# Optimization experiments

Hardware: AMD Instinct MI355X
Metric: run time of the kernel (lower is better)

The kernel has to match this reference:

```python
import jax, jax.numpy as jnp
from jax import lax
import numpy as np

B, L = 8, 2048
D_MODEL, D_STATE, D_CONV, EXPAND = 768, 16, 4, 2
D_INNER = EXPAND * D_MODEL          # 1536
DT_RANK = (D_MODEL + 15) // 16      # 48
OUT_DIM = 2


def setup_inputs() -> dict:
    key = jax.random.key(0)
    ks = jax.random.split(key, 10)
    rn = lambda k, sh, sc=0.02: jax.random.normal(k, sh, jnp.float32) * sc
    # S4D-real init for A_log, as in mamba_ssm
    A_log = jnp.log(jnp.broadcast_to(
        jnp.arange(1, D_STATE + 1, dtype=jnp.float32), (D_INNER, D_STATE)))
    return {
        "x": jax.random.normal(ks[0], (B, L, D_MODEL), jnp.float32),
        "in_proj_w": rn(ks[1], (2 * D_INNER, D_MODEL)),
        "conv_w": rn(ks[2], (D_INNER, D_CONV), 0.1),   # depthwise kernel
        "conv_b": jnp.zeros((D_INNER,), jnp.float32),
        "x_proj_w": rn(ks[3], (DT_RANK + 2 * D_STATE, D_INNER)),
        "dt_proj_w": rn(ks[4], (D_INNER, DT_RANK), 0.1),
        "dt_proj_b": rn(ks[5], (D_INNER,), 0.1),
        "A_log": A_log,
        "D": jnp.ones((D_INNER,), jnp.float32),
        "out_proj_w": rn(ks[6], (D_MODEL, D_INNER)),
        "fc_w": rn(ks[7], (OUT_DIM, D_MODEL)),
        "fc_b": jnp.zeros((OUT_DIM,), jnp.float32),
    }


def _mamba(x, in_proj_w, conv_w, conv_b, x_proj_w, dt_proj_w, dt_proj_b,
           A_log, D, out_proj_w):
    # input projection -> x branch and gate z, each [B, L, E]
    xz = jnp.einsum('bld,ed->ble', x, in_proj_w)
    xi, z = jnp.split(xz, 2, axis=-1)
    # causal depthwise conv1d over time, then SiLU
    xc = jnp.swapaxes(xi, 1, 2)                      # [B, E, L]
    xc = lax.conv_general_dilated(
        xc, conv_w[:, None, :], window_strides=(1,),
        padding=[(D_CONV - 1, 0)], feature_group_count=D_INNER)
    xi = jax.nn.silu(jnp.swapaxes(xc + conv_b[None, :, None], 1, 2))  # [B,L,E]
    # input-dependent dt, B, C
    dbc = jnp.einsum('ble,fe->blf', xi, x_proj_w)    # [B, L, R+2N]
    dt, Bm, Cm = jnp.split(dbc, [DT_RANK, DT_RANK + D_STATE], axis=-1)
    delta = jax.nn.softplus(jnp.einsum('blr,er->ble', dt, dt_proj_w) + dt_proj_b)
    A = -jnp.exp(A_log)                              # [E, N]

    def step(h, inputs):
        d_t, b_t, c_t, x_t = inputs                  # [B,E],[B,N],[B,N],[B,E]
        dA = jnp.exp(d_t[..., None] * A)             # [B, E, N]
        h = dA * h + (d_t * x_t)[..., None] * b_t[:, None, :]
        y = jnp.einsum('ben,bn->be', h, c_t)
        return h, y

    h0 = jnp.zeros((x.shape[0], D_INNER, D_STATE), x.dtype)
    xs = (jnp.swapaxes(delta, 0, 1), jnp.swapaxes(Bm, 0, 1),
          jnp.swapaxes(Cm, 0, 1), jnp.swapaxes(xi, 0, 1))
    _, ys = lax.scan(step, h0, xs)                   # ys: [L, B, E]
    y = jnp.swapaxes(ys, 0, 1) + xi * D
    y = y * jax.nn.silu(z)
    return jnp.einsum('ble,de->bld', y, out_proj_w)  # [B, L, d_model]


def reference(x, in_proj_w, conv_w, conv_b, x_proj_w, dt_proj_w, dt_proj_b,
              A_log, D, out_proj_w, fc_w, fc_b):
    out = _mamba(x, in_proj_w, conv_w, conv_b, x_proj_w, dt_proj_w,
                 dt_proj_b, A_log, D, out_proj_w)
    pooled = out.mean(axis=1)                        # [B, d_model]
    return pooled @ fc_w.T + fc_b                    # [B, OUT_DIM]
```

## Files before the change

kernel.cpp:

```cpp
#include <hip/hip_runtime.h>
#include <cstdint>
#include <cmath>

#define B_    8
#define L_    2048
#define DM    768
#define DI    1536
#define NX    3072
#define RK    48
#define DBCW  80
#define SB    2
#define NSLAB (B_/SB)
#define TS    (SB*L_)

typedef _Float16 f16;
typedef __attribute__((ext_vector_type(8))) _Float16 f16x8;
typedef __attribute__((ext_vector_type(4))) _Float16 f16x4;
typedef __attribute__((ext_vector_type(4))) float    f32x4;

__global__ void k_cvt_h(const float* __restrict__ in, f16* __restrict__ out, int n4) {
    int i = blockIdx.x * 256 + threadIdx.x;
    if (i >= n4) return;
    f32x4 v = *(const f32x4*)(in + (size_t)i * 4);
    f16x4 o;
#pragma unroll
    for (int j = 0; j < 4; ++j) o[j] = (f16)v[j];
    *(f16x4*)(out + (size_t)i * 4) = o;
}

__global__ void k_ws_dbg(float* out, float v) {
    if (threadIdx.x < 16) out[threadIdx.x] = v;
}

#define LDR 40
__global__ __launch_bounds__(256) void k_gemm1(const f16* __restrict__ Ah, const f16* __restrict__ Bw,
                                               f16* __restrict__ C) {
    __shared__ f16 lA[2][128 * LDR];
    __shared__ f16 lB[2][128 * LDR];
    const int tid  = threadIdx.x;
    const int lane = tid & 63;
    const int wave = tid >> 6;
    const int wm = wave >> 1, wn = wave & 1;
    const int row0 = blockIdx.x * 128;
    const int col0 = blockIdx.y * 128;
    const int fr = lane & 15;
    const int kg = lane >> 4;

    f32x4 acc[4][4] = {};

    const int s_r = tid >> 2;
    const int s_c = (tid & 3) * 8;
    const f16* gA0 = Ah + (size_t)(row0 + s_r)      * DM + s_c;
    const f16* gA1 = Ah + (size_t)(row0 + 64 + s_r) * DM + s_c;
    const f16* gB0 = Bw + (size_t)(col0 + s_r)      * DM + s_c;
    const f16* gB1 = Bw + (size_t)(col0 + 64 + s_r) * DM + s_c;
    const int ldso = s_r * LDR + s_c;

    f16x8 ra0 = *(const f16x8*)(gA0);
    f16x8 ra1 = *(const f16x8*)(gA1);
    f16x8 rb0 = *(const f16x8*)(gB0);
    f16x8 rb1 = *(const f16x8*)(gB1);
    *(f16x8*)(lA[0] + ldso) = ra0;
    *(f16x8*)(lA[0] + 64 * LDR + ldso) = ra1;
    *(f16x8*)(lB[0] + ldso) = rb0;
    *(f16x8*)(lB[0] + 64 * LDR + ldso) = rb1;

    const int NK = DM / 32;
    for (int t = 0; t < NK; ++t) {
        const int cur = t & 1;
        if (t + 1 < NK) {
            const int k0 = (t + 1) * 32;
            ra0 = *(const f16x8*)(gA0 + k0);
            ra1 = *(const f16x8*)(gA1 + k0);
            rb0 = *(const f16x8*)(gB0 + k0);
            rb1 = *(const f16x8*)(gB1 + k0);
        }
        __syncthreads();
        f16x8 af[4], bfv[4];
#pragma unroll
        for (int i = 0; i < 4; ++i)
            af[i] = *(const f16x8*)(lA[cur] + (wm * 64 + i * 16 + fr) * LDR + kg * 8);
#pragma unroll
        for (int j = 0; j < 4; ++j)
            bfv[j] = *(const f16x8*)(lB[cur] + (wn * 64 + j * 16 + fr) * LDR + kg * 8);
#pragma unroll
        for (int i = 0; i < 4; ++i)
#pragma unroll
            for (int j = 0; j < 4; ++j)
                acc[i][j] = __builtin_amdgcn_mfma_f32_16x16x32_f16(af[i], bfv[j], acc[i][j], 0, 0, 0);
        if (t + 1 < NK) {
            f16* dA = lA[cur ^ 1];
            f16* dB = lB[cur ^ 1];
            *(f16x8*)(dA + ldso) = ra0;
            *(f16x8*)(dA + 64 * LDR + ldso) = ra1;
            *(f16x8*)(dB + ldso) = rb0;
            *(f16x8*)(dB + 64 * LDR + ldso) = rb1;
        }
    }
#pragma unroll
    for (int i = 0; i < 4; ++i) {
        int r0 = row0 + wm * 64 + i * 16 + kg * 4;
#pragma unroll
        for (int j = 0; j < 4; ++j) {
            int c = col0 + wn * 64 + j * 16 + fr;
#pragma unroll
            for (int r = 0; r < 4; ++r)
                C[(size_t)(r0 + r) * NX + c] = (f16)acc[i][j][r];
        }
    }
}

__global__ void k_conv(const f16* __restrict__ xz, const float* __restrict__ cw,
                       const float* __restrict__ cb, f16* __restrict__ xi) {
    int idx = blockIdx.x * 256 + threadIdx.x;
    int ch4 = (idx % 384) * 4;
    int t   = idx / 384;
    if (t >= TS) return;
    int l = t & (L_ - 1);
    const f16* base = xz + (size_t)t * NX + ch4;
    f32x4 s = *(const f32x4*)(cb + ch4);
    f32x4 w0 = *(const f32x4*)(cw + (ch4 + 0) * 4);
    f32x4 w1 = *(const f32x4*)(cw + (ch4 + 1) * 4);
    f32x4 w2 = *(const f32x4*)(cw + (ch4 + 2) * 4);
    f32x4 w3 = *(const f32x4*)(cw + (ch4 + 3) * 4);
#pragma unroll
    for (int j = 0; j < 4; ++j) {
        if (l - 3 + j >= 0) {
            f16x4 v = *(const f16x4*)(base + (ptrdiff_t)(j - 3) * NX);
            s[0] += w0[j] * (float)v[0];
            s[1] += w1[j] * (float)v[1];
            s[2] += w2[j] * (float)v[2];
            s[3] += w3[j] * (float)v[3];
        }
    }
    f16x4 o;
#pragma unroll
    for (int c = 0; c < 4; ++c) {
        float x = s[c];
        o[c] = (f16)(x / (1.f + __expf(-x)));
    }
    *(f16x4*)(xi + (size_t)t * DI + ch4) = o;
}

__global__ __launch_bounds__(256) void k_gemm2(const f16* __restrict__ xi, const float* __restrict__ xw,
                                               float* __restrict__ dbc) {
    __shared__ f16 lA[64 * LDR];
    __shared__ f16 lB[80 * LDR];
    const int tid  = threadIdx.x;
    const int lane = tid & 63;
    const int wv   = tid >> 6;
    const int fr = lane & 15;
    const int kg = lane >> 4;
    const int t0 = blockIdx.x * 64;
    const int kbase = blockIdx.y * (DI / 2);

    f32x4 acc[5] = {};
    const int s_r = tid >> 2;
    const int s_c = (tid & 3) * 8;
    const f16* gA0 = xi + (size_t)(t0 + s_r) * DI + kbase + s_c;

    for (int k0 = 0; k0 < DI / 2; k0 += 32) {
        f16x8 va0 = *(const f16x8*)(gA0 + k0);
        int q0 = tid, q1 = tid + 256, q2 = tid + 512;
        f32x4 vb0 = *(const f32x4*)(xw + (size_t)(q0 >> 3) * DI + kbase + k0 + (q0 & 7) * 4);
        f32x4 vb1 = *(const f32x4*)(xw + (size_t)(q1 >> 3) * DI + kbase + k0 + (q1 & 7) * 4);
        f32x4 vb2;
        bool m2 = q2 < 640;
        if (m2) vb2 = *(const f32x4*)(xw + (size_t)(q2 >> 3) * DI + kbase + k0 + (q2 & 7) * 4);
        __syncthreads();
        *(f16x8*)(lA + s_r * LDR + s_c) = va0;
        {
            f16x4 h0, h1;
#pragma unroll
            for (int j = 0; j < 4; ++j) { h0[j] = (f16)vb0[j]; h1[j] = (f16)vb1[j]; }
            *(f16x4*)(lB + (q0 >> 3) * LDR + (q0 & 7) * 4) = h0;
            *(f16x4*)(lB + (q1 >> 3) * LDR + (q1 & 7) * 4) = h1;
            if (m2) {
                f16x4 h2;
#pragma unroll
                for (int j = 0; j < 4; ++j) h2[j] = (f16)vb2[j];
                *(f16x4*)(lB + (q2 >> 3) * LDR + (q2 & 7) * 4) = h2;
            }
        }
        __syncthreads();
        f16x8 af = *(const f16x8*)(lA + (wv * 16 + fr) * LDR + kg * 8);
        f16x8 bfv[5];
#pragma unroll
        for (int j = 0; j < 5; ++j)
            bfv[j] = *(const f16x8*)(lB + (j * 16 + fr) * LDR + kg * 8);
#pragma unroll
        for (int j = 0; j < 5; ++j)
            acc[j] = __builtin_amdgcn_mfma_f32_16x16x32_f16(af, bfv[j], acc[j], 0, 0, 0);
    }
    int r0 = t0 + wv * 16 + kg * 4;
#pragma unroll
    for (int j = 0; j < 5; ++j) {
        int c = j * 16 + fr;
#pragma unroll
        for (int r = 0; r < 4; ++r)
            atomicAdd(&dbc[(size_t)(r0 + r) * DBCW + c], acc[j][r]);
    }
}

#define G3_TT 32
__global__ __launch_bounds__(256) void k_gemm3(const float* __restrict__ dbc, const float* __restrict__ dw,
                                               const float* __restrict__ db, f16* __restrict__ delta) {
    __shared__ float dts[G3_TT * RK];
    int tid = threadIdx.x;
    int t0 = blockIdx.x * G3_TT;
    int e = blockIdx.y * 256 + tid;
    for (int q = tid; q < G3_TT * 12; q += 256) {
        int row = q / 12, c4 = (q % 12) * 4;
        *(f32x4*)(dts + row * RK + c4) = *(const f32x4*)(dbc + (size_t)(t0 + row) * DBCW + c4);
    }
    float wr[RK];
#pragma unroll
    for (int r4 = 0; r4 < 12; ++r4) {
        f32x4 v = *(const f32x4*)(dw + (size_t)e * RK + r4 * 4);
        wr[r4 * 4] = v[0]; wr[r4 * 4 + 1] = v[1]; wr[r4 * 4 + 2] = v[2]; wr[r4 * 4 + 3] = v[3];
    }
    float bias = db[e];
    __syncthreads();
    for (int tt = 0; tt < G3_TT; ++tt) {
        float s = bias;
#pragma unroll
        for (int r4 = 0; r4 < 12; ++r4) {
            f32x4 v = *(const f32x4*)(dts + tt * RK + r4 * 4);
            s += wr[r4 * 4] * v[0] + wr[r4 * 4 + 1] * v[1] + wr[r4 * 4 + 2] * v[2] + wr[r4 * 4 + 3] * v[3];
        }
        float sp = (s > 20.f) ? s : log1pf(__expf(s));
        delta[(size_t)(t0 + tt) * DI + e] = (f16)sp;
    }
}

__global__ __launch_bounds__(256) void k_scan1(const f16* __restrict__ xz, const f16* __restrict__ xi,
                                               const f16* __restrict__ delta, const float* __restrict__ dbc,
                                               const float* __restrict__ Dp,
                                               float* __restrict__ Ac, float* __restrict__ Bc,
                                               float* __restrict__ Gc, float* __restrict__ Sc,
                                               int clen) {
    __shared__ float bcs[16 * 32];
    __shared__ f16 xis[16 * 256], zsh[16 * 256], dsh[16 * 256];
    const int tid = threadIdx.x;
    const int e0 = blockIdx.x * 256, e = e0 + tid;
    const int c = blockIdx.y, bl = blockIdx.z;
    const int nch = gridDim.y;
    const float Dv = Dp[e];
    float h[16] = {}, P[16], G[16] = {};
    float S = 0.f;
#pragma unroll
    for (int n = 0; n < 16; ++n) P[n] = 1.f;
    const size_t tb0 = (size_t)bl * L_ + (size_t)c * clen;

    for (int g = 0; g < clen / 16; ++g) {
        size_t tb = tb0 + g * 16;
        if (tid < 128) {
            int row = tid >> 3, c4 = (tid & 7) * 4;
            *(f32x4*)(bcs + row * 32 + c4) = *(const f32x4*)(dbc + (tb + row) * DBCW + RK + c4);
        }
#pragma unroll
        for (int r = 0; r < 2; ++r) {
            int q = tid + 256 * r;
            int row = q >> 5, cc = (q & 31) * 8;
            *(f16x8*)(xis + row * 256 + cc) = *(const f16x8*)(xi    + (tb + row) * DI + e0 + cc);
            *(f16x8*)(zsh + row * 256 + cc) = *(const f16x8*)(xz    + (tb + row) * NX + DI + e0 + cc);
            *(f16x8*)(dsh + row * 256 + cc) = *(const f16x8*)(delta + (tb + row) * DI + e0 + cc);
        }
        __syncthreads();
        for (int s = 0; s < 16; ++s) {
            float Bv[16], Cv[16];
#pragma unroll
            for (int q = 0; q < 4; ++q) {
                *(f32x4*)&Bv[q * 4] = *(const f32x4*)(bcs + s * 32 + q * 4);
                *(f32x4*)&Cv[q * 4] = *(const f32x4*)(bcs + s * 32 + 16 + q * 4);
            }
            float d  = (float)dsh[s * 256 + tid];
            float xv = (float)xis[s * 256 + tid];
            float zv = (float)zsh[s * 256 + tid];
            float w = __expf(-d);
            float du = d * xv;
            float sg = zv / (1.f + __expf(-zv));
            float W[16];
            W[0] = w;           W[1] = w * w;       W[2] = W[1] * w;    W[3] = W[1] * W[1];
            W[4] = W[3] * w;    W[5] = W[3] * W[1]; W[6] = W[3] * W[2]; W[7] = W[3] * W[3];
            W[8] = W[7] * W[0]; W[9] = W[7] * W[1]; W[10] = W[7] * W[2]; W[11] = W[7] * W[3];
            W[12] = W[7] * W[4]; W[13] = W[7] * W[5]; W[14] = W[7] * W[6]; W[15] = W[7] * W[7];
            float y0 = 0.f, y1 = 0.f, y2 = 0.f, y3 = 0.f;
#pragma unroll
            for (int n = 0; n < 16; n += 4) {
                h[n]     = W[n]     * h[n]     + du * Bv[n];
                h[n + 1] = W[n + 1] * h[n + 1] + du * Bv[n + 1];
                h[n + 2] = W[n + 2] * h[n + 2] + du * Bv[n + 2];
                h[n + 3] = W[n + 3] * h[n + 3] + du * Bv[n + 3];
                y0 += h[n] * Cv[n];
                y1 += h[n + 1] * Cv[n + 1];
                y2 += h[n + 2] * Cv[n + 2];
                y3 += h[n + 3] * Cv[n + 3];
                P[n]     *= W[n];
                P[n + 1] *= W[n + 1];
                P[n + 2] *= W[n + 2];
                P[n + 3] *= W[n + 3];
                G[n]     += sg * Cv[n] * P[n];
                G[n + 1] += sg * Cv[n + 1] * P[n + 1];
                G[n + 2] += sg * Cv[n + 2] * P[n + 2];
                G[n + 3] += sg * Cv[n + 3] * P[n + 3];
            }
            S += sg * (((y0 + y1) + (y2 + y3)) + xv * Dv);
        }
        __syncthreads();
    }
    size_t o = (((size_t)bl * nch + c) * DI + e) * 16;
#pragma unroll
    for (int q = 0; q < 4; ++q) {
        f32x4 vp = {P[4 * q], P[4 * q + 1], P[4 * q + 2], P[4 * q + 3]};
        f32x4 vh = {h[4 * q], h[4 * q + 1], h[4 * q + 2], h[4 * q + 3]};
        f32x4 vg = {G[4 * q], G[4 * q + 1], G[4 * q + 2], G[4 * q + 3]};
        *(f32x4*)(Ac + o + 4 * q) = vp;
        *(f32x4*)(Bc + o + 4 * q) = vh;
        *(f32x4*)(Gc + o + 4 * q) = vg;
    }
    Sc[((size_t)bl * nch + c) * DI + e] = S;
}

__global__ __launch_bounds__(256) void k_scan2(const float* __restrict__ Ac, const float* __restrict__ Bc,
                                               const float* __restrict__ Gc, const float* __restrict__ Sc,
                                               float* __restrict__ py, int gb0, int nch) {
    const int tid = threadIdx.x;
    const int n = tid & 15;
    const int e = blockIdx.x * 16 + (tid >> 4);
    const int bl = blockIdx.y;
    float h0 = 0.f, r = 0.f;
    for (int c = 0; c < nch; ++c) {
        size_t o = (((size_t)bl * nch + c) * DI + e) * 16 + n;
        r += Gc[o] * h0;
        h0 = Ac[o] * h0 + Bc[o];
    }
#pragma unroll
    for (int m = 1; m < 16; m <<= 1) r += __shfl_xor(r, m, 64);
    if (n == 0) {
        float ss = 0.f;
        for (int c = 0; c < nch; ++c) ss += Sc[((size_t)bl * nch + c) * DI + e];
        py[(size_t)(gb0 + bl) * DI + e] = (r + ss) * (1.f / (float)L_);
    }
}

__global__ __launch_bounds__(256) void k_mat(const float* __restrict__ fw, const float* __restrict__ opw,
                                             float* __restrict__ M) {
    int e = blockIdx.x * 256 + threadIdx.x;
    int o = blockIdx.y;
    float acc = 0.f;
    for (int d = 0; d < DM; ++d)
        acc += fw[o * DM + d] * opw[(size_t)d * DI + e];
    M[o * DI + e] = acc;
}

__global__ __launch_bounds__(256) void k_fc2(const float* __restrict__ py, const float* __restrict__ M,
                                             const float* __restrict__ fb, float* __restrict__ out) {
    int tid = threadIdx.x;
    int p = tid >> 4;
    int lane16 = tid & 15;
    int b = p >> 1, o = p & 1;
    float acc = 0.f;
    for (int k = lane16; k < DI; k += 16)
        acc += py[(size_t)b * DI + k] * M[o * DI + k];
#pragma unroll
    for (int m = 1; m < 16; m <<= 1) acc += __shfl_xor(acc, m, 64);
    if (lane16 == 0) out[b * 2 + o] = acc + fb[o];
}

extern "C" void kernel_launch(void* const* d_in, const int* in_sizes, int n_in,
                              void* d_out, int out_size, void* d_ws, size_t ws_size,
                              hipStream_t stream) {
    const float* x    = (const float*)d_in[0];
    const float* ipw  = (const float*)d_in[1];
    const float* cw   = (const float*)d_in[2];
    const float* cb   = (const float*)d_in[3];
    const float* xpw  = (const float*)d_in[4];
    const float* dpw  = (const float*)d_in[5];
    const float* dpb  = (const float*)d_in[6];
    const float* Dp   = (const float*)d_in[8];
    const float* opw  = (const float*)d_in[9];
    const float* fw   = (const float*)d_in[10];
    const float* fb   = (const float*)d_in[11];
    float* out = (float*)d_out;

    char* wsb = (char*)d_ws;
    size_t off = 0;
    auto alloc = [&](size_t bytes) -> void* {
        void* p = wsb + off;
        off = (off + bytes + 255) & ~(size_t)255;
        return p;
    };
    f16*   wbf   = (f16*)alloc((size_t)NX * DM * 2);
    f16*   xz    = (f16*)alloc((size_t)TS * NX * 2);
    f16*   xi    = (f16*)alloc((size_t)TS * DI * 2);
    f16*   delta = (f16*)alloc((size_t)TS * DI * 2);
    float* dbc   = (float*)alloc((size_t)TS * DBCW * 4);
    float* py    = (float*)alloc((size_t)B_ * DI * 4);
    float* M     = (float*)alloc((size_t)2 * DI * 4);
    int nch = 64;
    size_t base = off;
    float *Ac = nullptr, *Bc = nullptr, *Gc = nullptr, *Sc = nullptr;
    for (;; nch >>= 1) {
        off = base;
        Ac = (float*)alloc((size_t)SB * nch * DI * 16 * 4);
        Bc = (float*)alloc((size_t)SB * nch * DI * 16 * 4);
        Gc = (float*)alloc((size_t)SB * nch * DI * 16 * 4);
        Sc = (float*)alloc((size_t)SB * nch * DI * 4);
        if (off <= ws_size) break;
        if (nch == 16) {
            k_ws_dbg<<<1, 16, 0, stream>>>(out, (float)ws_size);
            return;
        }
    }
    const int clen = L_ / nch;
    f16* xh = delta;

    int n4w = NX * DM / 4;
    k_cvt_h<<<(n4w + 255) / 256, 256, 0, stream>>>(ipw, wbf, n4w);
    dim3 gm(DI / 256, 2);
    k_mat<<<gm, 256, 0, stream>>>(fw, opw, M);

    for (int s = 0; s < NSLAB; ++s) {
        int tok0 = s * TS;
        int n4x = TS * DM / 4;
        k_cvt_h<<<(n4x + 255) / 256, 256, 0, stream>>>(x + (size_t)tok0 * DM, xh, n4x);
        dim3 g1(TS / 128, NX / 128);
        k_gemm1<<<g1, 256, 0, stream>>>(xh, wbf, xz);
        k_conv<<<TS * 384 / 256, 256, 0, stream>>>(xz, cw, cb, xi);
        hipMemsetAsync(dbc, 0, (size_t)TS * DBCW * 4, stream);
        dim3 g2g(TS / 64, 2);
        k_gemm2<<<g2g, 256, 0, stream>>>(xi, xpw, dbc);
        dim3 g3(TS / G3_TT, 6);
        k_gemm3<<<g3, 256, 0, stream>>>(dbc, dpw, dpb, delta);
        dim3 gs(DI / 256, nch, SB);
        k_scan1<<<gs, 256, 0, stream>>>(xz, xi, delta, dbc, Dp, Ac, Bc, Gc, Sc, clen);
        dim3 g2(DI / 16, SB);
        k_scan2<<<g2, 256, 0, stream>>>(Ac, Bc, Gc, Sc, py, s * SB, nch);
    }
    k_fc2<<<1, 256, 0, stream>>>(py, M, fb, out);
}
```

Measured before the change: 854.4 us.

## Fuse input fp32-to-fp16 conversion into gemm1, remap tiles, parallelize chunk scan

The activation fp32-to-fp16 conversion kernel is removed and folded into gemm1's global loads, which now read fp32 x directly and convert in registers. Gemm1 tiles are also remapped so consecutive blocks spread across column tiles, which should help cache locality. The cross-chunk combine in scan2 moves from a serial loop over chunks to a warp-level parallel prefix scan, with one wavefront per channel and chunks held in lanes. In exchange, gemm1 loads twice as many bytes for A, and scan2 does more shuffle work and holds more registers.

Measured after the change: 799.0 us. 1.07x faster.

```diff
diff --git a/kernel.cpp b/kernel.cpp
--- a/kernel.cpp
+++ b/kernel.cpp
@@ -33,16 +33,18 @@
 }
 
 #define LDR 40
-__global__ __launch_bounds__(256) void k_gemm1(const f16* __restrict__ Ah, const f16* __restrict__ Bw,
-                                               f16* __restrict__ C) {
+__global__ __launch_bounds__(256) void k_gemm1(const float* __restrict__ X, const f16* __restrict__ Bw,
+                                               f16* __restrict__ C, int tok0) {
     __shared__ f16 lA[2][128 * LDR];
     __shared__ f16 lB[2][128 * LDR];
     const int tid  = threadIdx.x;
     const int lane = tid & 63;
     const int wave = tid >> 6;
     const int wm = wave >> 1, wn = wave & 1;
-    const int row0 = blockIdx.x * 128;
-    const int col0 = blockIdx.y * 128;
+    const int d  = blockIdx.y * 32 + blockIdx.x;
+    const int t_ = (d & 7) * 96 + (d >> 3);
+    const int row0 = (t_ & 31) * 128;
+    const int col0 = (t_ >> 5) * 128;
     const int fr = lane & 15;
     const int kg = lane >> 4;
 
@@ -50,14 +52,21 @@
 
     const int s_r = tid >> 2;
     const int s_c = (tid & 3) * 8;
-    const f16* gA0 = Ah + (size_t)(row0 + s_r)      * DM + s_c;
-    const f16* gA1 = Ah + (size_t)(row0 + 64 + s_r) * DM + s_c;
-    const f16* gB0 = Bw + (size_t)(col0 + s_r)      * DM + s_c;
-    const f16* gB1 = Bw + (size_t)(col0 + 64 + s_r) * DM + s_c;
+    const float* gA0 = X + (size_t)(tok0 + row0 + s_r)      * DM + s_c;
+    const float* gA1 = X + (size_t)(tok0 + row0 + 64 + s_r) * DM + s_c;
+    const f16*   gB0 = Bw + (size_t)(col0 + s_r)      * DM + s_c;
+    const f16*   gB1 = Bw + (size_t)(col0 + 64 + s_r) * DM + s_c;
     const int ldso = s_r * LDR + s_c;
 
-    f16x8 ra0 = *(const f16x8*)(gA0);
-    f16x8 ra1 = *(const f16x8*)(gA1);
+    auto cvt8 = [](f32x4 lo, f32x4 hi) {
+        f16x8 h;
+#pragma unroll
+        for (int j = 0; j < 4; ++j) { h[j] = (f16)lo[j]; h[4 + j] = (f16)hi[j]; }
+        return h;
+    };
+
+    f16x8 ra0 = cvt8(*(const f32x4*)(gA0), *(const f32x4*)(gA0 + 4));
+    f16x8 ra1 = cvt8(*(const f32x4*)(gA1), *(const f32x4*)(gA1 + 4));
     f16x8 rb0 = *(const f16x8*)(gB0);
     f16x8 rb1 = *(const f16x8*)(gB1);
     *(f16x8*)(lA[0] + ldso) = ra0;
@@ -70,8 +79,8 @@
         const int cur = t & 1;
         if (t + 1 < NK) {
             const int k0 = (t + 1) * 32;
-            ra0 = *(const f16x8*)(gA0 + k0);
-            ra1 = *(const f16x8*)(gA1 + k0);
+            ra0 = cvt8(*(const f32x4*)(gA0 + k0), *(const f32x4*)(gA0 + k0 + 4));
+            ra1 = cvt8(*(const f32x4*)(gA1 + k0), *(const f32x4*)(gA1 + k0 + 4));
             rb0 = *(const f16x8*)(gB0 + k0);
             rb1 = *(const f16x8*)(gB1 + k0);
         }
@@ -325,23 +334,48 @@
 __global__ __launch_bounds__(256) void k_scan2(const float* __restrict__ Ac, const float* __restrict__ Bc,
                                                const float* __restrict__ Gc, const float* __restrict__ Sc,
                                                float* __restrict__ py, int gb0, int nch) {
-    const int tid = threadIdx.x;
-    const int n = tid & 15;
-    const int e = blockIdx.x * 16 + (tid >> 4);
+    const int tid  = threadIdx.x;
+    const int lane = tid & 63;
+    const int e  = blockIdx.x * 4 + (tid >> 6);
     const int bl = blockIdx.y;
-    float h0 = 0.f, r = 0.f;
-    for (int c = 0; c < nch; ++c) {
-        size_t o = (((size_t)bl * nch + c) * DI + e) * 16 + n;
-        r += Gc[o] * h0;
-        h0 = Ac[o] * h0 + Bc[o];
-    }
-#pragma unroll
-    for (int m = 1; m < 16; m <<= 1) r += __shfl_xor(r, m, 64);
-    if (n == 0) {
-        float ss = 0.f;
-        for (int c = 0; c < nch; ++c) ss += Sc[((size_t)bl * nch + c) * DI + e];
-        py[(size_t)(gb0 + bl) * DI + e] = (r + ss) * (1.f / (float)L_);
-    }
+    float A[16], Bv[16], G[16];
+    float Sv = 0.f;
+    if (lane < nch) {
+        size_t o = (((size_t)bl * nch + lane) * DI + e) * 16;
+#pragma unroll
+        for (int q = 0; q < 4; ++q) {
+            *(f32x4*)&A[q * 4]  = *(const f32x4*)(Ac + o + q * 4);
+            *(f32x4*)&Bv[q * 4] = *(const f32x4*)(Bc + o + q * 4);
+            *(f32x4*)&G[q * 4]  = *(const f32x4*)(Gc + o + q * 4);
+        }
+        Sv = Sc[((size_t)bl * nch + lane) * DI + e];
+    } else {
+#pragma unroll
+        for (int n = 0; n < 16; ++n) { A[n] = 1.f; Bv[n] = 0.f; G[n] = 0.f; }
+    }
+#pragma unroll
+    for (int d_ = 1; d_ < 64; d_ <<= 1) {
+#pragma unroll
+        for (int n = 0; n < 16; ++n) {
+            float Au = __shfl_up(A[n],  d_, 64);
+            float Bu = __shfl_up(Bv[n], d_, 64);
+            Au = (lane >= d_) ? Au : 1.f;
+            Bu = (lane >= d_) ? Bu : 0.f;
+            Bv[n] = A[n] * Bu + Bv[n];
+            A[n]  = A[n] * Au;
+        }
+    }
+    float r = 0.f;
+#pragma unroll
+    for (int n = 0; n < 16; ++n) {
+        float h0 = __shfl_up(Bv[n], 1, 64);
+        h0 = (lane == 0) ? 0.f : h0;
+        r += G[n] * h0;
+    }
+    r += Sv;
+#pragma unroll
+    for (int m = 1; m < 64; m <<= 1) r += __shfl_xor(r, m, 64);
+    if (lane == 0) py[(size_t)(gb0 + bl) * DI + e] = r * (1.f / (float)L_);
 }
 
 __global__ __launch_bounds__(256) void k_mat(const float* __restrict__ fw, const float* __restrict__ opw,
@@ -414,7 +448,6 @@
         }
     }
     const int clen = L_ / nch;
-    f16* xh = delta;
 
     int n4w = NX * DM / 4;
     k_cvt_h<<<(n4w + 255) / 256, 256, 0, stream>>>(ipw, wbf, n4w);
@@ -423,10 +456,8 @@
 
     for (int s = 0; s < NSLAB; ++s) {
         int tok0 = s * TS;
-        int n4x = TS * DM / 4;
-        k_cvt_h<<<(n4x + 255) / 256, 256, 0, stream>>>(x + (size_t)tok0 * DM, xh, n4x);
-        dim3 g1(TS / 128, NX / 128);
-        k_gemm1<<<g1, 256, 0, stream>>>(xh, wbf, xz);
+        dim3 g1(32, NX / 128);
+        k_gemm1<<<g1, 256, 0, stream>>>(x, wbf, xz, tok0);
         k_conv<<<TS * 384 / 256, 256, 0, stream>>>(xz, cw, cb, xi);
         hipMemsetAsync(dbc, 0, (size_t)TS * DBCW * 4, stream);
         dim3 g2g(TS / 64, 2);
@@ -435,7 +466,7 @@
         k_gemm3<<<g3, 256, 0, stream>>>(dbc, dpw, dpb, delta);
         dim3 gs(DI / 256, nch, SB);
         k_scan1<<<gs, 256, 0, stream>>>(xz, xi, delta, dbc, Dp, Ac, Bc, Gc, Sc, clen);
-        dim3 g2(DI / 16, SB);
+        dim3 g2(DI / 4, SB);
         k_scan2<<<g2, 256, 0, stream>>>(Ac, Bc, Gc, Sc, py, s * SB, nch);
     }
     k_fc2<<<1, 256, 0, stream>>>(py, M, fb, out);
```
